# Kernel optimization log

Hardware: AMD Instinct MI355X
Metric: run time of the kernel (lower is better)

## Reference

```python
import jax, jax.numpy as jnp
import numpy as np

DEPTH = 5
B, CHANNELS, LENGTH = 256, 10, 128


def setup_inputs() -> dict:
    key = jax.random.key(0)
    # torch module convention: (batch, channels, length); transposed internally to (length, channels)
    path = jax.random.normal(key, (B, CHANNELS, LENGTH), dtype=jnp.float32)
    return {"path": path, "depth": DEPTH}


def _seg_levels(delta, depth):
    # Signature of a single linear segment with increment delta: level k = delta^{\otimes k} / k!
    # delta: (B, d) -> list of (B, d**k) for k = 1..depth
    b = delta.shape[0]
    levels = [delta]
    cur = delta
    for k in range(2, depth + 1):
        cur = (cur[:, :, None] * delta[:, None, :]).reshape(b, -1) / k
        levels.append(cur)
    return levels


def _signature(path_ld, depth):
    # path_ld: (B, L, d) piecewise-linear path; returns (B, sum_k d**k)
    b, L, d = path_ld.shape
    inc = path_ld[:, 1:] - path_ld[:, :-1]  # (B, L-1, d) segment increments
    init = tuple(_seg_levels(inc[:, 0], depth))

    def step(carry, delta):
        # Chen's relation: (S \otimes T)_k = S_k + T_k + sum_{i=1}^{k-1} S_i \otimes T_{k-i}
        T = _seg_levels(delta, depth)
        new = []
        for k in range(1, depth + 1):
            acc = carry[k - 1] + T[k - 1]
            for i in range(1, k):
                acc = acc + (carry[i - 1][:, :, None] * T[k - i - 1][:, None, :]).reshape(b, d ** k)
            new.append(acc)
        return tuple(new), None

    deltas = jnp.swapaxes(inc[:, 1:], 0, 1)  # (L-2, B, d) remaining segments
    final, _ = jax.lax.scan(step, init, deltas)
    return jnp.concatenate(final, axis=-1)


def reference(path, depth):
    # path: (B, channels, length) as in the torch module; iisignature sees (length, channels)
    return _signature(jnp.swapaxes(path, 1, 2), depth)
```

## Files before the change

kernel.cpp:

```cpp
#include <hip/hip_runtime.h>


#define D10    10
#define LPATH  128
#define NSEG   127
#define BLOCK  512
#define NROW   256
#define NROWA  250
#define NCOL   112
#define NCOLA  110
#define KC     16
#define NCH    8
#define SD     132
#define OUT_PER_B 111110

typedef __attribute__((ext_vector_type(8))) short bf16x8;
typedef __attribute__((ext_vector_type(4))) float f32x4;

__device__ __forceinline__ unsigned pack_split(float x, float y, unsigned &lo)
{
    unsigned xb = __float_as_uint(x), yb = __float_as_uint(y);
    float xr = x - __uint_as_float(xb & 0xffff0000u);
    float yr = y - __uint_as_float(yb & 0xffff0000u);
    lo = (__float_as_uint(xr) >> 16) | (__float_as_uint(yr) & 0xffff0000u);
    return (xb >> 16) | (yb & 0xffff0000u);
}

__global__ __launch_bounds__(BLOCK, 1) void sig_kernel(
        const float* __restrict__ path,
        float* __restrict__ out)
{
    __shared__ __align__(16) float dTT[D10 * SD];
    __shared__ __align__(16) float RT [D10 * SD];
    __shared__ __align__(16) short AhiS[2][4 * NROW * 8];
    __shared__ __align__(16) short AloS[2][4 * NROW * 8];
    __shared__ __align__(16) short BhiS[2][4 * NCOL * 8];
    __shared__ __align__(16) short BloS[2][4 * NCOL * 8];

    const int tid = threadIdx.x;
    const int bb  = blockIdx.x;
    const int b   = bb >> 2;
    const int q   = bb & 3;
    const float* pb = path + (size_t)b * (D10 * LPATH);

    for (int idx = tid; idx < D10 * SD; idx += BLOCK) {
        int c = idx / SD, t = idx - c * SD;
        float d = 0.f, r = 0.f;
        if (t < NSEG) {
            float p1 = pb[c * LPATH + t + 1];
            d = p1 - pb[c * LPATH + t];
            r = pb[c * LPATH + NSEG] - p1;
        }
        dTT[idx] = d;
        RT [idx] = r;
    }
    for (int idx = tid; idx < 2 * 4 * (NROW - NROWA) * 8; idx += BLOCK) {
        int bufi = idx / (4 * 6 * 8);
        int rem  = idx - bufi * (4 * 6 * 8);
        int kg   = rem / (6 * 8);
        int rr   = rem - kg * (6 * 8);
        int o = (kg * NROW + NROWA) * 8 + rr;
        AhiS[bufi][o] = 0; AloS[bufi][o] = 0;
    }
    if (tid < 2 * 4 * 2 * 8) {
        int bufi = tid >> 6;
        int rem  = tid & 63;
        int kg   = rem >> 4;
        int rr   = rem & 15;
        int o = (kg * NCOL + NCOLA) * 8 + rr;
        BhiS[bufi][o] = 0; BloS[bufi][o] = 0;
    }

    const int grow = q * NROWA + tid;
    const int g   = grow / 100;
    const int m3  = grow - g * 100;
    const int c2  = m3 / 10;
    const int c3  = m3 - c2 * 10;
    const int goff = g * SD, c2off = c2 * SD, c3off = c3 * SD;

    const int lane = tid & 63;
    const int wv   = tid >> 6;
    const int rl   = lane & 15;
    const int kgl  = lane >> 4;

    float s1 = 0.f, s2 = 0.f, s3 = 0.f;
    f32x4 acc[2][7];
#pragma unroll
    for (int i = 0; i < 2; ++i)
#pragma unroll
        for (int nt = 0; nt < 7; ++nt) acc[i][nt] = f32x4{0.f, 0.f, 0.f, 0.f};

    auto produce = [&](int pp, int kc0) {
        if (tid < NROWA) {
#pragma unroll
            for (int w0 = 0; w0 < KC; w0 += 4) {
                float4 g4 = *(const float4*)&dTT[goff  + kc0 + w0];
                float4 a4 = *(const float4*)&dTT[c2off + kc0 + w0];
                float4 b4 = *(const float4*)&dTT[c3off + kc0 + w0];
                float ga[4] = {g4.x, g4.y, g4.z, g4.w};
                float aa[4] = {a4.x, a4.y, a4.z, a4.w};
                float ba[4] = {b4.x, b4.y, b4.z, b4.w};
                unsigned hw[4], lw[4];
#pragma unroll
                for (int j = 0; j < 4; ++j) {
                    float dg = ga[j], d2 = aa[j], d3 = ba[j];
                    float u24 = s2 + (s1 + dg * 0.25f)     * d2 * (1.f / 3.f);
                    float u25 = s2 + (s1 + dg * 0.2f)      * d2 * 0.25f;
                    float u23 = s2 + (s1 + dg * (1.f/3.f)) * d2 * 0.5f;
                    float w1v = s3 + u24 * d3 * 0.5f;
                    float w0h = 0.5f * (s3 + u25 * d3 * (1.f / 3.f));
                    s3 += u23 * d3;
                    s2 += (s1 + dg * 0.5f) * d2;
                    s1 += dg;
                    hw[j] = pack_split(w1v, w0h, lw[j]);
                }
                const int ai = ((w0 >> 2) * NROW + tid) * 8;
                *(uint4*)&AhiS[pp][ai] = make_uint4(hw[0], hw[1], hw[2], hw[3]);
                *(uint4*)&AloS[pp][ai] = make_uint4(lw[0], lw[1], lw[2], lw[3]);
            }
        } else if (tid >= 256) {
            for (int s = tid - 256; s < 4 * NCOLA; s += 256) {
                const int cb  = s >> 2;
                const int kgB = s & 3;
                int c4o, ebo = 0;
                if (cb < 100) { int c4 = cb / 10; ebo = (cb - c4 * 10) * SD; c4o = c4 * SD; }
                else          { c4o = (cb - 100) * SD; }
                const int u0 = kc0 + kgB * 4;
                float4 d4 = *(const float4*)&dTT[c4o + u0];
                float da[4] = {d4.x, d4.y, d4.z, d4.w};
                unsigned hw[4], lw[4];
                if (cb < 100) {
                    float4 e4 = *(const float4*)&dTT[ebo + u0];
                    float4 r4 = *(const float4*)&RT [ebo + u0];
                    float ea[4] = {e4.x, e4.y, e4.z, e4.w};
                    float ra[4] = {r4.x, r4.y, r4.z, r4.w};
#pragma unroll
                    for (int j = 0; j < 4; ++j)
                        hw[j] = pack_split(da[j] * ra[j], da[j] * ea[j], lw[j]);
                } else {
#pragma unroll
                    for (int j = 0; j < 4; ++j)
                        hw[j] = pack_split(da[j], 0.f, lw[j]);
                }
                const int bi = (kgB * NCOL + cb) * 8;
                *(uint4*)&BhiS[pp][bi] = make_uint4(hw[0], hw[1], hw[2], hw[3]);
                *(uint4*)&BloS[pp][bi] = make_uint4(lw[0], lw[1], lw[2], lw[3]);
            }
        }
    };

    __syncthreads();
    produce(0, 0);
    __syncthreads();

    for (int ch = 0; ch < NCH; ++ch) {
        const int p = ch & 1;
        bf16x8 bh[7], bl[7];
#pragma unroll
        for (int nt = 0; nt < 7; ++nt) {
            const int bi = (kgl * NCOL + nt * 16 + rl) * 8;
            bh[nt] = *(const bf16x8*)&BhiS[p][bi];
            bl[nt] = *(const bf16x8*)&BloS[p][bi];
        }
        bf16x8 ah[2], al[2];
#pragma unroll
        for (int i = 0; i < 2; ++i) {
            const int ai = (kgl * NROW + wv * 32 + i * 16 + rl) * 8;
            ah[i] = *(const bf16x8*)&AhiS[p][ai];
            al[i] = *(const bf16x8*)&AloS[p][ai];
        }
        if (ch + 1 < NCH) produce(p ^ 1, (ch + 1) * KC);
#pragma unroll
        for (int i = 0; i < 2; ++i)
#pragma unroll
            for (int nt = 0; nt < 7; ++nt) {
                acc[i][nt] = __builtin_amdgcn_mfma_f32_16x16x32_bf16(ah[i], bh[nt], acc[i][nt], 0, 0, 0);
                acc[i][nt] = __builtin_amdgcn_mfma_f32_16x16x32_bf16(ah[i], bl[nt], acc[i][nt], 0, 0, 0);
                acc[i][nt] = __builtin_amdgcn_mfma_f32_16x16x32_bf16(al[i], bh[nt], acc[i][nt], 0, 0, 0);
                acc[i][nt] = __builtin_amdgcn_mfma_f32_16x16x32_bf16(al[i], bl[nt], acc[i][nt], 0, 0, 0);
            }
        __syncthreads();
    }

    float* ob = out + (size_t)b * OUT_PER_B;
    if (tid < NROWA) {
        ob[110 + grow] = s3;
        if (c3 == 0) ob[10 + g * 10 + c2] = s2;
        if (m3 == 0) ob[g] = s1;
    }
#pragma unroll
    for (int i = 0; i < 2; ++i) {
#pragma unroll
        for (int r = 0; r < 4; ++r) {
            const int prow = wv * 32 + i * 16 + kgl * 4 + r;
            if (prow < NROWA) {
                const int gr = q * NROWA + prow;
#pragma unroll
                for (int nt = 0; nt < 7; ++nt) {
                    const int col = nt * 16 + rl;
                    const float v = acc[i][nt][r];
                    if (col < 100)
                        ob[11110 + (size_t)gr * 100 + col] = v;
                    else if (col < NCOLA)
                        ob[1110 + gr * 10 + (col - 100)] = v;
                }
            }
        }
    }
}

extern "C" void kernel_launch(void* const* d_in, const int* in_sizes, int n_in,
                              void* d_out, int out_size, void* d_ws, size_t ws_size,
                              hipStream_t stream) {
    const float* path = (const float*)d_in[0];
    float* out = (float*)d_out;
    int B = in_sizes[0] / (D10 * LPATH);
    sig_kernel<<<B * 4, BLOCK, 0, stream>>>(path, out);
}
```

Baseline: 193.0 us.

## Split each batch row across eight blocks with one MFMA row tile per wave

Each batch element now spans 8 blocks of 125 rows instead of 4 blocks of 250. Each wave computes one 16-row tile instead of two, and B fragments are loaded per column tile instead of all at once. The single-block-per-CU launch bound is dropped, so register use falls and more blocks can be resident. The cost is twice as many blocks redundantly loading the path and building the shared B operand, plus fewer MFMAs per block to hide the producer work.

New measurement: 241.6 us. 1.25x slower.

```diff
diff --git a/kernel.cpp b/kernel.cpp
--- a/kernel.cpp
+++ b/kernel.cpp
@@ -5,8 +5,8 @@
 #define LPATH  128
 #define NSEG   127
 #define BLOCK  512
-#define NROW   256
-#define NROWA  250
+#define NROW   128
+#define NROWA  125
 #define NCOL   112
 #define NCOLA  110
 #define KC     16
@@ -26,7 +26,7 @@
     return (xb >> 16) | (yb & 0xffff0000u);
 }
 
-__global__ __launch_bounds__(BLOCK, 1) void sig_kernel(
+__global__ __launch_bounds__(BLOCK) void sig_kernel(
         const float* __restrict__ path,
         float* __restrict__ out)
 {
@@ -39,8 +39,8 @@
 
     const int tid = threadIdx.x;
     const int bb  = blockIdx.x;
-    const int b   = bb >> 2;
-    const int q   = bb & 3;
+    const int b   = bb >> 3;
+    const int q   = bb & 7;
     const float* pb = path + (size_t)b * (D10 * LPATH);
 
     for (int idx = tid; idx < D10 * SD; idx += BLOCK) {
@@ -55,10 +55,10 @@
         RT [idx] = r;
     }
     for (int idx = tid; idx < 2 * 4 * (NROW - NROWA) * 8; idx += BLOCK) {
-        int bufi = idx / (4 * 6 * 8);
-        int rem  = idx - bufi * (4 * 6 * 8);
-        int kg   = rem / (6 * 8);
-        int rr   = rem - kg * (6 * 8);
+        int bufi = idx / (4 * (NROW - NROWA) * 8);
+        int rem  = idx - bufi * (4 * (NROW - NROWA) * 8);
+        int kg   = rem / ((NROW - NROWA) * 8);
+        int rr   = rem - kg * ((NROW - NROWA) * 8);
         int o = (kg * NROW + NROWA) * 8 + rr;
         AhiS[bufi][o] = 0; AloS[bufi][o] = 0;
     }
@@ -84,11 +84,9 @@
     const int kgl  = lane >> 4;
 
     float s1 = 0.f, s2 = 0.f, s3 = 0.f;
-    f32x4 acc[2][7];
-#pragma unroll
-    for (int i = 0; i < 2; ++i)
-#pragma unroll
-        for (int nt = 0; nt < 7; ++nt) acc[i][nt] = f32x4{0.f, 0.f, 0.f, 0.f};
+    f32x4 acc[7];
+#pragma unroll
+    for (int nt = 0; nt < 7; ++nt) acc[nt] = f32x4{0.f, 0.f, 0.f, 0.f};
 
     auto produce = [&](int pp, int kc0) {
         if (tid < NROWA) {
@@ -118,8 +116,8 @@
                 *(uint4*)&AhiS[pp][ai] = make_uint4(hw[0], hw[1], hw[2], hw[3]);
                 *(uint4*)&AloS[pp][ai] = make_uint4(lw[0], lw[1], lw[2], lw[3]);
             }
-        } else if (tid >= 256) {
-            for (int s = tid - 256; s < 4 * NCOLA; s += 256) {
+        } else if (tid >= 128) {
+            for (int s = tid - 128; s < 4 * NCOLA; s += 384) {
                 const int cb  = s >> 2;
                 const int kgB = s & 3;
                 int c4o, ebo = 0;
@@ -155,30 +153,20 @@
 
     for (int ch = 0; ch < NCH; ++ch) {
         const int p = ch & 1;
-        bf16x8 bh[7], bl[7];
+        const int ai = (kgl * NROW + wv * 16 + rl) * 8;
+        bf16x8 ah = *(const bf16x8*)&AhiS[p][ai];
+        bf16x8 al = *(const bf16x8*)&AloS[p][ai];
+        if (ch + 1 < NCH) produce(p ^ 1, (ch + 1) * KC);
 #pragma unroll
         for (int nt = 0; nt < 7; ++nt) {
             const int bi = (kgl * NCOL + nt * 16 + rl) * 8;
-            bh[nt] = *(const bf16x8*)&BhiS[p][bi];
-            bl[nt] = *(const bf16x8*)&BloS[p][bi];
-        }
-        bf16x8 ah[2], al[2];
-#pragma unroll
-        for (int i = 0; i < 2; ++i) {
-            const int ai = (kgl * NROW + wv * 32 + i * 16 + rl) * 8;
-            ah[i] = *(const bf16x8*)&AhiS[p][ai];
-            al[i] = *(const bf16x8*)&AloS[p][ai];
-        }
-        if (ch + 1 < NCH) produce(p ^ 1, (ch + 1) * KC);
-#pragma unroll
-        for (int i = 0; i < 2; ++i)
-#pragma unroll
-            for (int nt = 0; nt < 7; ++nt) {
-                acc[i][nt] = __builtin_amdgcn_mfma_f32_16x16x32_bf16(ah[i], bh[nt], acc[i][nt], 0, 0, 0);
-                acc[i][nt] = __builtin_amdgcn_mfma_f32_16x16x32_bf16(ah[i], bl[nt], acc[i][nt], 0, 0, 0);
-                acc[i][nt] = __builtin_amdgcn_mfma_f32_16x16x32_bf16(al[i], bh[nt], acc[i][nt], 0, 0, 0);
-                acc[i][nt] = __builtin_amdgcn_mfma_f32_16x16x32_bf16(al[i], bl[nt], acc[i][nt], 0, 0, 0);
-            }
+            bf16x8 bh = *(const bf16x8*)&BhiS[p][bi];
+            bf16x8 bl = *(const bf16x8*)&BloS[p][bi];
+            acc[nt] = __builtin_amdgcn_mfma_f32_16x16x32_bf16(ah, bh, acc[nt], 0, 0, 0);
+            acc[nt] = __builtin_amdgcn_mfma_f32_16x16x32_bf16(ah, bl, acc[nt], 0, 0, 0);
+            acc[nt] = __builtin_amdgcn_mfma_f32_16x16x32_bf16(al, bh, acc[nt], 0, 0, 0);
+            acc[nt] = __builtin_amdgcn_mfma_f32_16x16x32_bf16(al, bl, acc[nt], 0, 0, 0);
+        }
         __syncthreads();
     }
 
@@ -189,21 +177,18 @@
         if (m3 == 0) ob[g] = s1;
     }
 #pragma unroll
-    for (int i = 0; i < 2; ++i) {
-#pragma unroll
-        for (int r = 0; r < 4; ++r) {
-            const int prow = wv * 32 + i * 16 + kgl * 4 + r;
-            if (prow < NROWA) {
-                const int gr = q * NROWA + prow;
-#pragma unroll
-                for (int nt = 0; nt < 7; ++nt) {
-                    const int col = nt * 16 + rl;
-                    const float v = acc[i][nt][r];
-                    if (col < 100)
-                        ob[11110 + (size_t)gr * 100 + col] = v;
-                    else if (col < NCOLA)
-                        ob[1110 + gr * 10 + (col - 100)] = v;
-                }
+    for (int r = 0; r < 4; ++r) {
+        const int prow = wv * 16 + kgl * 4 + r;
+        if (prow < NROWA) {
+            const int gr = q * NROWA + prow;
+#pragma unroll
+            for (int nt = 0; nt < 7; ++nt) {
+                const int col = nt * 16 + rl;
+                const float v = acc[nt][r];
+                if (col < 100)
+                    ob[11110 + (size_t)gr * 100 + col] = v;
+                else if (col < NCOLA)
+                    ob[1110 + gr * 10 + (col - 100)] = v;
             }
         }
     }
@@ -215,5 +200,5 @@
     const float* path = (const float*)d_in[0];
     float* out = (float*)d_out;
     int B = in_sizes[0] / (D10 * LPATH);
-    sig_kernel<<<B * 4, BLOCK, 0, stream>>>(path, out);
+    sig_kernel<<<B * 8, BLOCK, 0, stream>>>(path, out);
 }
```
